# Optimization experiments

Hardware: AMD Instinct MI355X
Metric: run time of the kernel (lower is better)

The kernel has to match this reference:

```python
import jax, jax.numpy as jnp
import numpy as np

N, D_IN, D_OUT = 4096, 1024, 1024

def setup_inputs() -> dict:
    key = jax.random.key(0)
    k1, k2, k3, k4 = jax.random.split(key, 4)
    x = jax.random.normal(k1, (N, D_IN), dtype=jnp.float32)
    # original uses torch.rand (uniform [0,1)) for params
    w_query = jax.random.uniform(k2, (D_IN, D_OUT), dtype=jnp.float32)
    w_key = jax.random.uniform(k3, (D_IN, D_OUT), dtype=jnp.float32)
    w_value = jax.random.uniform(k4, (D_IN, D_OUT), dtype=jnp.float32)
    return {"x": x, "w_query": w_query, "w_key": w_key, "w_value": w_value}

def reference(x, w_query, w_key, w_value):
    queries = x @ w_query          # [N, d_out]
    keys = x @ w_key               # [N, d_out]
    values = x @ w_value           # [N, d_out]
    scale = keys.shape[-1] ** 0.5
    scores = queries @ keys.T      # [N, N]
    attn = jax.nn.softmax(scores / scale, axis=-1)
    return attn @ values           # [N, d_out]
```

## Files before the change

### kernel.cpp

```cpp
#include <hip/hip_runtime.h>
#include <math.h>

#define NROWS 4096
#define DDIM  1024

typedef __attribute__((ext_vector_type(8))) short short8;
typedef __attribute__((ext_vector_type(4))) float f32x4;

__device__ __forceinline__ ushort f2bf(float v) {
  union { float f; uint32_t u; } c; c.f = v;
  uint32_t u = c.u;
  uint32_t lsb = (u >> 16) & 1u;
  u += 0x7fffu + lsb;
  return (ushort)(u >> 16);
}
__device__ __forceinline__ float bf2f(ushort h) {
  union { uint32_t u; float f; } c; c.u = ((uint32_t)h) << 16;
  return c.f;
}

__device__ __forceinline__ void gll16(const void* g, void* l) {
  __builtin_amdgcn_global_load_lds((const __attribute__((address_space(1))) void*)g,
                                   (__attribute__((address_space(3))) void*)l, 16, 0, 0);
}

__device__ __forceinline__ size_t pidx(int r, int c, int ldt) {
  return ((size_t)((r >> 4) * ldt + (c >> 5))) * 512 +
         ((c >> 3) & 3) * 128 + (r & 15) * 8 + (c & 7);
}

__global__ __launch_bounds__(256) void prep(const float* __restrict__ x,
                                            const float* __restrict__ wq,
                                            const float* __restrict__ wk,
                                            const float* __restrict__ wv,
                                            ushort* Xh, ushort* Xl,
                                            ushort* Wqh, ushort* Wql,
                                            ushort* Wkh, ushort* Wkl, ushort* Wvh) {
  __shared__ float tl[32][33];
  const int b = blockIdx.x, t = threadIdx.x;
  if (b < 1024) {
    const float4* src = (const float4*)x;
    ushort4* hi = (ushort4*)Xh;
    ushort4* lo = (ushort4*)Xl;
#pragma unroll
    for (int r = 0; r < 4; ++r) {
      int i = b * 1024 + r * 256 + t;
      float4 v = src[i];
      ushort4 h, l;
      h.x = f2bf(v.x); l.x = f2bf(v.x - bf2f(h.x));
      h.y = f2bf(v.y); l.y = f2bf(v.y - bf2f(h.y));
      h.z = f2bf(v.z); l.z = f2bf(v.z - bf2f(h.z));
      h.w = f2bf(v.w); l.w = f2bf(v.w - bf2f(h.w));
      hi[i] = h; lo[i] = l;
    }
  } else {
    const int z = (b - 1024) >> 10;
    const int tile = (b - 1024) & 1023;
    const float* src = z == 0 ? wq : (z == 1 ? wk : wv);
    ushort* dh = z == 0 ? Wqh : (z == 1 ? Wkh : Wvh);
    ushort* dl = z == 0 ? Wql : (z == 1 ? Wkl : nullptr);
    const int r0 = (tile >> 5) * 32;
    const int c0 = (tile & 31) * 32;
    const int tx = t & 31, ty = t >> 5;
    for (int i = ty; i < 32; i += 8)
      tl[i][tx] = src[(size_t)(r0 + i) * DDIM + c0 + tx];
    __syncthreads();
    for (int i = ty; i < 32; i += 8) {
      float v = tl[tx][i];
      ushort h = f2bf(v);
      size_t o = (size_t)(c0 + i) * DDIM + r0 + tx;
      dh[o] = h;
      if (dl) dl[o] = f2bf(v - bf2f(h));
    }
  }
}

template <int BM, bool SPLIT>
__device__ __forceinline__ void gemm_core(const ushort* __restrict__ Ah,
                                          const ushort* __restrict__ Al,
                                          const ushort* __restrict__ Bh,
                                          const ushort* __restrict__ Bl,
                                          int lda, int ldb, int kbeg, int kend,
                                          int m0, int n0, ushort* sm,
                                          f32x4 (*acc)[4]) {
  constexpr int MI = BM / 32;
  constexpr int ATILE = BM * 32;
  constexpr int BTILE = 128 * 32;
  ushort* sAh = sm;
  ushort* sAl = SPLIT ? sm + ATILE : nullptr;
  ushort* sBh = sm + (SPLIT ? 2 * ATILE : ATILE);
  ushort* sBl = SPLIT ? sBh + BTILE : nullptr;

  const int t = threadIdx.x;
  const int wv = t >> 6, ln = t & 63;
  const int quad = ln >> 4, l16 = ln & 15;
  const int key = (l16 >> 1) & 3;
  const int arb = (wv >> 1) * (BM / 2);
  const int crb = (wv & 1) * 64;

  for (int k0 = kbeg; k0 < kend; k0 += 32) {
#pragma unroll
    for (int r = 0; r < BM * 64 / 4096; ++r) {
      int f = t * 16 + r * 4096;
      int row = f >> 6;
      int srcq = ((f >> 4) & 3) ^ ((row >> 1) & 3);
      size_t go = (size_t)(m0 + row) * lda + k0 + srcq * 8;
      gll16(Ah + go, sAh + (f >> 1));
      if (SPLIT) gll16(Al + go, sAl + (f >> 1));
    }
#pragma unroll
    for (int r = 0; r < 2; ++r) {
      int f = t * 16 + r * 4096;
      int row = f >> 6;
      int srcq = ((f >> 4) & 3) ^ ((row >> 1) & 3);
      size_t go = (size_t)(n0 + row) * ldb + k0 + srcq * 8;
      gll16(Bh + go, sBh + (f >> 1));
      if (SPLIT) gll16(Bl + go, sBl + (f >> 1));
    }
    __syncthreads();

    short8 ah[MI], bh[4], al[MI], bl[4];
#pragma unroll
    for (int i = 0; i < MI; ++i) {
      int off = (arb + i * 16 + l16) * 32 + (quad ^ key) * 8;
      ah[i] = *(const short8*)(sAh + off);
      if (SPLIT) al[i] = *(const short8*)(sAl + off);
    }
#pragma unroll
    for (int j = 0; j < 4; ++j) {
      int off = (crb + j * 16 + l16) * 32 + (quad ^ key) * 8;
      bh[j] = *(const short8*)(sBh + off);
      if (SPLIT) bl[j] = *(const short8*)(sBl + off);
    }
#pragma unroll
    for (int i = 0; i < MI; ++i)
#pragma unroll
      for (int j = 0; j < 4; ++j) {
        acc[i][j] = __builtin_amdgcn_mfma_f32_16x16x32_bf16(ah[i], bh[j], acc[i][j], 0, 0, 0);
        if (SPLIT) {
          acc[i][j] = __builtin_amdgcn_mfma_f32_16x16x32_bf16(ah[i], bl[j], acc[i][j], 0, 0, 0);
          acc[i][j] = __builtin_amdgcn_mfma_f32_16x16x32_bf16(al[i], bh[j], acc[i][j], 0, 0, 0);
        }
      }
    __syncthreads();
  }
}

__global__ __launch_bounds__(256) void gemm_qkv(const ushort* __restrict__ Xh,
                                                const ushort* __restrict__ Xl,
                                                const ushort* __restrict__ Wqh, const ushort* __restrict__ Wql,
                                                const ushort* __restrict__ Wkh, const ushort* __restrict__ Wkl,
                                                const ushort* __restrict__ Wvh,
                                                ushort* Qh, ushort* Ql, ushort* Kh, ushort* Kl, ushort* Vt) {
  extern __shared__ ushort sm[];
  const int which = blockIdx.x % 3;
  const int g = blockIdx.x / 3;
  const int t = threadIdx.x;
  const int wv = t >> 6, ln = t & 63;
  const int quad = ln >> 4, l16 = ln & 15;

  f32x4 acc[4][4];
#pragma unroll
  for (int i = 0; i < 4; ++i)
#pragma unroll
    for (int j = 0; j < 4; ++j) acc[i][j] = (f32x4){0.f, 0.f, 0.f, 0.f};

  if (which == 2) {
    const int m0 = g * 128;
    const int n0 = blockIdx.y * 128;
    gemm_core<128, false>(Wvh, nullptr, Xh, nullptr, DDIM, DDIM, 0, DDIM, m0, n0, sm, acc);
#pragma unroll
    for (int i = 0; i < 4; ++i)
#pragma unroll
      for (int j = 0; j < 4; ++j) {
        int kv = n0 + (wv & 1) * 64 + j * 16 + l16;
        int d = m0 + (wv >> 1) * 64 + i * 16 + quad * 4;
#pragma unroll
        for (int r2 = 0; r2 < 4; ++r2)
          Vt[pidx(d + r2, kv, NROWS / 32)] = f2bf(acc[i][j][r2]);
      }
  } else {
    const int n0 = g * 128;
    const int m0 = blockIdx.y * 128;
    const ushort* Bh = which ? Wkh : Wqh;
    const ushort* Bl = which ? Wkl : Wql;
    gemm_core<128, true>(Xh, Xl, Bh, Bl, DDIM, DDIM, 0, DDIM, m0, n0, sm, acc);
    const float scale = which ? 1.0f : 0.03125f;
    ushort* H = which ? Kh : Qh;
    ushort* L = which ? Kl : Ql;
#pragma unroll
    for (int i = 0; i < 4; ++i)
#pragma unroll
      for (int j = 0; j < 4; ++j) {
        int col = n0 + (wv & 1) * 64 + j * 16 + l16;
        int rw = m0 + (wv >> 1) * 64 + i * 16 + quad * 4;
#pragma unroll
        for (int r2 = 0; r2 < 4; ++r2) {
          float v = acc[i][j][r2] * scale;
          ushort h = f2bf(v);
          size_t o = pidx(rw + r2, col, DDIM / 32);
          H[o] = h;
          L[o] = f2bf(v - bf2f(h));
        }
      }
  }
}

__global__ __launch_bounds__(256) void gemm_s(const ushort* __restrict__ Qh, const ushort* __restrict__ Ql,
                                              const ushort* __restrict__ Kh, const ushort* __restrict__ Kl,
                                              float* __restrict__ S) {
  const int n0 = blockIdx.x * 128, m0 = blockIdx.y * 128;
  const int t = threadIdx.x;
  const int wv = t >> 6, ln = t & 63;
  const int quad = ln >> 4, l16 = ln & 15;
  const int arb = (wv >> 1) * 64, crb = (wv & 1) * 64;
  const int ra = (m0 + arb) >> 4;
  const int rb = (n0 + crb) >> 4;

  f32x4 acc[4][4];
#pragma unroll
  for (int i = 0; i < 4; ++i)
#pragma unroll
    for (int j = 0; j < 4; ++j) acc[i][j] = (f32x4){0.f, 0.f, 0.f, 0.f};

  size_t baseA[4], baseB[4];
#pragma unroll
  for (int i = 0; i < 4; ++i) baseA[i] = (size_t)(ra + i) * 16384 + ln * 8;
#pragma unroll
  for (int j = 0; j < 4; ++j) baseB[j] = (size_t)(rb + j) * 16384 + ln * 8;

#pragma unroll 2
  for (int s = 0; s < 32; ++s) {
    short8 ah[4], al[4];
#pragma unroll
    for (int i = 0; i < 4; ++i) {
      size_t o = baseA[i] + (size_t)s * 512;
      ah[i] = *(const short8*)(Qh + o);
      al[i] = *(const short8*)(Ql + o);
    }
#pragma unroll
    for (int j = 0; j < 4; ++j) {
      size_t o = baseB[j] + (size_t)s * 512;
      short8 bh = *(const short8*)(Kh + o);
      short8 bl = *(const short8*)(Kl + o);
#pragma unroll
      for (int i = 0; i < 4; ++i) {
        acc[i][j] = __builtin_amdgcn_mfma_f32_16x16x32_bf16(ah[i], bh, acc[i][j], 0, 0, 0);
        acc[i][j] = __builtin_amdgcn_mfma_f32_16x16x32_bf16(ah[i], bl, acc[i][j], 0, 0, 0);
        acc[i][j] = __builtin_amdgcn_mfma_f32_16x16x32_bf16(al[i], bh, acc[i][j], 0, 0, 0);
      }
    }
  }

#pragma unroll
  for (int i = 0; i < 4; ++i)
#pragma unroll
    for (int j = 0; j < 4; ++j) {
      int col = n0 + crb + j * 16 + l16;
      int rw = m0 + arb + i * 16 + quad * 4;
#pragma unroll
      for (int r2 = 0; r2 < 4; ++r2)
        S[(size_t)(rw + r2) * NROWS + col] = acc[i][j][r2];
    }
}

__global__ __launch_bounds__(256) void softmax_pack(const float* __restrict__ S,
                                                    ushort* __restrict__ P) {
  const int row = blockIdx.x, t = threadIdx.x;
  const float* Sr = S + (size_t)row * NROWS;
  const float4* S4 = (const float4*)Sr;
  float4 v[4];
  float mx = -3.4e38f;
#pragma unroll
  for (int c = 0; c < 4; ++c) {
    v[c] = S4[c * 256 + t];
    mx = fmaxf(mx, fmaxf(fmaxf(v[c].x, v[c].y), fmaxf(v[c].z, v[c].w)));
  }
  __shared__ float red[4];
  for (int o = 32; o >= 1; o >>= 1) mx = fmaxf(mx, __shfl_xor(mx, o));
  int wv = t >> 6, ln = t & 63;
  if (ln == 0) red[wv] = mx;
  __syncthreads();
  mx = fmaxf(fmaxf(red[0], red[1]), fmaxf(red[2], red[3]));
  float s = 0.f;
#pragma unroll
  for (int c = 0; c < 4; ++c) {
    v[c].x = __expf(v[c].x - mx);
    v[c].y = __expf(v[c].y - mx);
    v[c].z = __expf(v[c].z - mx);
    v[c].w = __expf(v[c].w - mx);
    s += v[c].x + v[c].y + v[c].z + v[c].w;
  }
  for (int o = 32; o >= 1; o >>= 1) s += __shfl_xor(s, o);
  __syncthreads();
  if (ln == 0) red[wv] = s;
  __syncthreads();
  s = red[0] + red[1] + red[2] + red[3];
  float inv = 1.f / s;
#pragma unroll
  for (int c = 0; c < 4; ++c) {
    ushort4 h;
    h.x = f2bf(v[c].x * inv);
    h.y = f2bf(v[c].y * inv);
    h.z = f2bf(v[c].z * inv);
    h.w = f2bf(v[c].w * inv);
    int c0 = 1024 * c + 4 * t;
    *(ushort4*)(P + pidx(row, c0, NROWS / 32)) = h;
  }
}

__global__ __launch_bounds__(256) void gemm_pv(const ushort* __restrict__ P,
                                               const ushort* __restrict__ Vt,
                                               float* __restrict__ Out) {
  const int n0 = blockIdx.x * 128, m0 = blockIdx.y * 64;
  const int t = threadIdx.x;
  const int wv = t >> 6, ln = t & 63;
  const int quad = ln >> 4, l16 = ln & 15;
  const int arb = (wv >> 1) * 32, crb = (wv & 1) * 64;
  const int ra = (m0 + arb) >> 4;
  const int rb = (n0 + crb) >> 4;

  f32x4 acc[2][4];
#pragma unroll
  for (int i = 0; i < 2; ++i)
#pragma unroll
    for (int j = 0; j < 4; ++j) acc[i][j] = (f32x4){0.f, 0.f, 0.f, 0.f};

  size_t baseA[2], baseB[4];
#pragma unroll
  for (int i = 0; i < 2; ++i) baseA[i] = (size_t)(ra + i) * 65536 + ln * 8;
#pragma unroll
  for (int j = 0; j < 4; ++j) baseB[j] = (size_t)(rb + j) * 65536 + ln * 8;

#pragma unroll 2
  for (int s = 0; s < 128; ++s) {
    short8 a0 = *(const short8*)(P + baseA[0] + (size_t)s * 512);
    short8 a1 = *(const short8*)(P + baseA[1] + (size_t)s * 512);
#pragma unroll
    for (int j = 0; j < 4; ++j) {
      short8 b = *(const short8*)(Vt + baseB[j] + (size_t)s * 512);
      acc[0][j] = __builtin_amdgcn_mfma_f32_16x16x32_bf16(a0, b, acc[0][j], 0, 0, 0);
      acc[1][j] = __builtin_amdgcn_mfma_f32_16x16x32_bf16(a1, b, acc[1][j], 0, 0, 0);
    }
  }

#pragma unroll
  for (int i = 0; i < 2; ++i)
#pragma unroll
    for (int j = 0; j < 4; ++j) {
      int col = n0 + crb + j * 16 + l16;
      int rw = m0 + arb + i * 16 + quad * 4;
#pragma unroll
      for (int r2 = 0; r2 < 4; ++r2)
        Out[(size_t)(rw + r2) * DDIM + col] = acc[i][j][r2];
    }
}

extern "C" void kernel_launch(void* const* d_in, const int* in_sizes, int n_in,
                              void* d_out, int out_size, void* d_ws, size_t ws_size,
                              hipStream_t stream) {
  const float* x  = (const float*)d_in[0];
  const float* wq = (const float*)d_in[1];
  const float* wk = (const float*)d_in[2];
  const float* wv = (const float*)d_in[3];
  char* ws = (char*)d_ws;
  const size_t MB = 1u << 20;

  ushort* Vt  = (ushort*)(ws + 0);
  ushort* Qh  = (ushort*)(ws + 8 * MB);
  ushort* Ql  = (ushort*)(ws + 16 * MB);
  ushort* Kh  = (ushort*)(ws + 24 * MB);
  ushort* Kl  = (ushort*)(ws + 32 * MB);
  ushort* Pp  = (ushort*)(ws + 8 * MB);
  ushort* Xh  = (ushort*)(ws + 40 * MB);
  ushort* Xl  = (ushort*)(ws + 48 * MB);
  ushort* Wqh = (ushort*)(ws + 56 * MB);
  ushort* Wql = (ushort*)(ws + 58 * MB);
  ushort* Wkh = (ushort*)(ws + 60 * MB);
  ushort* Wkl = (ushort*)(ws + 62 * MB);
  ushort* Wvh = (ushort*)(ws + 64 * MB);
  float*  S   = (float*)(ws + 40 * MB);
  float*  Out = (float*)d_out;

  prep<<<4096, 256, 0, stream>>>(x, wq, wk, wv, Xh, Xl, Wqh, Wql, Wkh, Wkl, Wvh);
  gemm_qkv<<<dim3(24, 32), 256, 32768, stream>>>(Xh, Xl, Wqh, Wql, Wkh, Wkl, Wvh,
                                                 Qh, Ql, Kh, Kl, Vt);
  gemm_s<<<dim3(32, 32), 256, 0, stream>>>(Qh, Ql, Kh, Kl, S);
  softmax_pack<<<NROWS, 256, 0, stream>>>(S, Pp);
  gemm_pv<<<dim3(8, 64), 256, 0, stream>>>(Pp, Vt, Out);
}
```

Before: 346.6 us.

## Pre-pack X and W into MFMA tile layout and use direct-load GEMM everywhere

```diff
diff --git a/kernel.cpp b/kernel.cpp
--- a/kernel.cpp
+++ b/kernel.cpp
@@ -17,11 +17,6 @@
 __device__ __forceinline__ float bf2f(ushort h) {
   union { uint32_t u; float f; } c; c.u = ((uint32_t)h) << 16;
   return c.f;
-}
-
-__device__ __forceinline__ void gll16(const void* g, void* l) {
-  __builtin_amdgcn_global_load_lds((const __attribute__((address_space(1))) void*)g,
-                                   (__attribute__((address_space(3))) void*)l, 16, 0, 0);
 }
 
 __device__ __forceinline__ size_t pidx(int r, int c, int ldt) {
@@ -40,18 +35,20 @@
   const int b = blockIdx.x, t = threadIdx.x;
   if (b < 1024) {
     const float4* src = (const float4*)x;
-    ushort4* hi = (ushort4*)Xh;
-    ushort4* lo = (ushort4*)Xl;
 #pragma unroll
     for (int r = 0; r < 4; ++r) {
       int i = b * 1024 + r * 256 + t;
+      int row = i >> 8;
+      int c = (i & 255) << 2;
       float4 v = src[i];
       ushort4 h, l;
       h.x = f2bf(v.x); l.x = f2bf(v.x - bf2f(h.x));
       h.y = f2bf(v.y); l.y = f2bf(v.y - bf2f(h.y));
       h.z = f2bf(v.z); l.z = f2bf(v.z - bf2f(h.z));
       h.w = f2bf(v.w); l.w = f2bf(v.w - bf2f(h.w));
-      hi[i] = h; lo[i] = l;
+      size_t o = pidx(row, c, DDIM / 32);
+      *(ushort4*)(Xh + o) = h;
+      *(ushort4*)(Xl + o) = l;
     }
   } else {
     const int z = (b - 1024) >> 10;
@@ -68,81 +65,57 @@
     for (int i = ty; i < 32; i += 8) {
       float v = tl[tx][i];
       ushort h = f2bf(v);
-      size_t o = (size_t)(c0 + i) * DDIM + r0 + tx;
+      size_t o = pidx(c0 + i, r0 + tx, DDIM / 32);
       dh[o] = h;
       if (dl) dl[o] = f2bf(v - bf2f(h));
     }
   }
 }
 
-template <int BM, bool SPLIT>
-__device__ __forceinline__ void gemm_core(const ushort* __restrict__ Ah,
-                                          const ushort* __restrict__ Al,
-                                          const ushort* __restrict__ Bh,
-                                          const ushort* __restrict__ Bl,
-                                          int lda, int ldb, int kbeg, int kend,
-                                          int m0, int n0, ushort* sm,
-                                          f32x4 (*acc)[4]) {
-  constexpr int MI = BM / 32;
-  constexpr int ATILE = BM * 32;
-  constexpr int BTILE = 128 * 32;
-  ushort* sAh = sm;
-  ushort* sAl = SPLIT ? sm + ATILE : nullptr;
-  ushort* sBh = sm + (SPLIT ? 2 * ATILE : ATILE);
-  ushort* sBl = SPLIT ? sBh + BTILE : nullptr;
-
+template <bool SPLIT, int KT>
+__device__ __forceinline__ void direct_gemm(const ushort* __restrict__ Ah,
+                                            const ushort* __restrict__ Al,
+                                            const ushort* __restrict__ Bh,
+                                            const ushort* __restrict__ Bl,
+                                            int m0, int n0, f32x4 (*acc)[4]) {
   const int t = threadIdx.x;
   const int wv = t >> 6, ln = t & 63;
-  const int quad = ln >> 4, l16 = ln & 15;
-  const int key = (l16 >> 1) & 3;
-  const int arb = (wv >> 1) * (BM / 2);
-  const int crb = (wv & 1) * 64;
-
-  for (int k0 = kbeg; k0 < kend; k0 += 32) {
-#pragma unroll
-    for (int r = 0; r < BM * 64 / 4096; ++r) {
-      int f = t * 16 + r * 4096;
-      int row = f >> 6;
-      int srcq = ((f >> 4) & 3) ^ ((row >> 1) & 3);
-      size_t go = (size_t)(m0 + row) * lda + k0 + srcq * 8;
-      gll16(Ah + go, sAh + (f >> 1));
-      if (SPLIT) gll16(Al + go, sAl + (f >> 1));
-    }
-#pragma unroll
-    for (int r = 0; r < 2; ++r) {
-      int f = t * 16 + r * 4096;
-      int row = f >> 6;
-      int srcq = ((f >> 4) & 3) ^ ((row >> 1) & 3);
-      size_t go = (size_t)(n0 + row) * ldb + k0 + srcq * 8;
-      gll16(Bh + go, sBh + (f >> 1));
-      if (SPLIT) gll16(Bl + go, sBl + (f >> 1));
-    }
-    __syncthreads();
-
-    short8 ah[MI], bh[4], al[MI], bl[4];
-#pragma unroll
-    for (int i = 0; i < MI; ++i) {
-      int off = (arb + i * 16 + l16) * 32 + (quad ^ key) * 8;
-      ah[i] = *(const short8*)(sAh + off);
-      if (SPLIT) al[i] = *(const short8*)(sAl + off);
+  const int arb = (wv >> 1) * 64, crb = (wv & 1) * 64;
+  const int ra = (m0 + arb) >> 4;
+  const int rb = (n0 + crb) >> 4;
+  const size_t ts = (size_t)KT * 512;
+
+  size_t baseA[4], baseB[4];
+#pragma unroll
+  for (int i = 0; i < 4; ++i) baseA[i] = (size_t)(ra + i) * ts + ln * 8;
+#pragma unroll
+  for (int j = 0; j < 4; ++j) baseB[j] = (size_t)(rb + j) * ts + ln * 8;
+
+#pragma unroll 2
+  for (int s = 0; s < KT; ++s) {
+    short8 ah[4], al[4];
+#pragma unroll
+    for (int i = 0; i < 4; ++i) {
+      size_t o = baseA[i] + (size_t)s * 512;
+      ah[i] = *(const short8*)(Ah + o);
+      if constexpr (SPLIT) al[i] = *(const short8*)(Al + o);
     }
 #pragma unroll
     for (int j = 0; j < 4; ++j) {
-      int off = (crb + j * 16 + l16) * 32 + (quad ^ key) * 8;
-      bh[j] = *(const short8*)(sBh + off);
-      if (SPLIT) bl[j] = *(const short8*)(sBl + off);
-    }
-#pragma unroll
-    for (int i = 0; i < MI; ++i)
-#pragma unroll
-      for (int j = 0; j < 4; ++j) {
-        acc[i][j] = __builtin_amdgcn_mfma_f32_16x16x32_bf16(ah[i], bh[j], acc[i][j], 0, 0, 0);
-        if (SPLIT) {
-          acc[i][j] = __builtin_amdgcn_mfma_f32_16x16x32_bf16(ah[i], bl[j], acc[i][j], 0, 0, 0);
-          acc[i][j] = __builtin_amdgcn_mfma_f32_16x16x32_bf16(al[i], bh[j], acc[i][j], 0, 0, 0);
+      size_t o = baseB[j] + (size_t)s * 512;
+      short8 bh = *(const short8*)(Bh + o);
+#pragma unroll
+      for (int i = 0; i < 4; ++i)
+        acc[i][j] = __builtin_amdgcn_mfma_f32_16x16x32_bf16(ah[i], bh, acc[i][j], 0, 0, 0);
+      if constexpr (SPLIT) {
+        short8 bl = *(const short8*)(Bl + o);
+#pragma unroll
+        for (int i = 0; i < 4; ++i) {
+          acc[i][j] = __builtin_amdgcn_mfma_f32_16x16x32_bf16(ah[i], bl, acc[i][j], 0, 0, 0);
+          acc[i][j] = __builtin_amdgcn_mfma_f32_16x16x32_bf16(al[i], bh, acc[i][j], 0, 0, 0);
         }
       }
-    __syncthreads();
+    }
   }
 }
 
@@ -152,9 +125,9 @@
                                                 const ushort* __restrict__ Wkh, const ushort* __restrict__ Wkl,
                                                 const ushort* __restrict__ Wvh,
                                                 ushort* Qh, ushort* Ql, ushort* Kh, ushort* Kl, ushort* Vt) {
-  extern __shared__ ushort sm[];
   const int which = blockIdx.x % 3;
   const int g = blockIdx.x / 3;
+  const int by = blockIdx.y;
   const int t = threadIdx.x;
   const int wv = t >> 6, ln = t & 63;
   const int quad = ln >> 4, l16 = ln & 15;
@@ -167,8 +140,8 @@
 
   if (which == 2) {
     const int m0 = g * 128;
-    const int n0 = blockIdx.y * 128;
-    gemm_core<128, false>(Wvh, nullptr, Xh, nullptr, DDIM, DDIM, 0, DDIM, m0, n0, sm, acc);
+    const int n0 = by * 128;
+    direct_gemm<false, DDIM / 32>(Wvh, nullptr, Xh, nullptr, m0, n0, acc);
 #pragma unroll
     for (int i = 0; i < 4; ++i)
 #pragma unroll
@@ -181,10 +154,10 @@
       }
   } else {
     const int n0 = g * 128;
-    const int m0 = blockIdx.y * 128;
+    const int m0 = by * 128;
     const ushort* Bh = which ? Wkh : Wqh;
     const ushort* Bl = which ? Wkl : Wql;
-    gemm_core<128, true>(Xh, Xl, Bh, Bl, DDIM, DDIM, 0, DDIM, m0, n0, sm, acc);
+    direct_gemm<true, DDIM / 32>(Xh, Xl, Bh, Bl, m0, n0, acc);
     const float scale = which ? 1.0f : 0.03125f;
     ushort* H = which ? Kh : Qh;
     ushort* L = which ? Kl : Ql;
@@ -213,9 +186,6 @@
   const int t = threadIdx.x;
   const int wv = t >> 6, ln = t & 63;
   const int quad = ln >> 4, l16 = ln & 15;
-  const int arb = (wv >> 1) * 64, crb = (wv & 1) * 64;
-  const int ra = (m0 + arb) >> 4;
-  const int rb = (n0 + crb) >> 4;
 
   f32x4 acc[4][4];
 #pragma unroll
@@ -223,41 +193,14 @@
 #pragma unroll
     for (int j = 0; j < 4; ++j) acc[i][j] = (f32x4){0.f, 0.f, 0.f, 0.f};
 
-  size_t baseA[4], baseB[4];
-#pragma unroll
-  for (int i = 0; i < 4; ++i) baseA[i] = (size_t)(ra + i) * 16384 + ln * 8;
-#pragma unroll
-  for (int j = 0; j < 4; ++j) baseB[j] = (size_t)(rb + j) * 16384 + ln * 8;
-
-#pragma unroll 2
-  for (int s = 0; s < 32; ++s) {
-    short8 ah[4], al[4];
-#pragma unroll
-    for (int i = 0; i < 4; ++i) {
-      size_t o = baseA[i] + (size_t)s * 512;
-      ah[i] = *(const short8*)(Qh + o);
-      al[i] = *(const short8*)(Ql + o);
-    }
+  direct_gemm<true, DDIM / 32>(Qh, Ql, Kh, Kl, m0, n0, acc);
+
+#pragma unroll
+  for (int i = 0; i < 4; ++i)
 #pragma unroll
     for (int j = 0; j < 4; ++j) {
-      size_t o = baseB[j] + (size_t)s * 512;
-      short8 bh = *(const short8*)(Kh + o);
-      short8 bl = *(const short8*)(Kl + o);
-#pragma unroll
-      for (int i = 0; i < 4; ++i) {
-        acc[i][j] = __builtin_amdgcn_mfma_f32_16x16x32_bf16(ah[i], bh, acc[i][j], 0, 0, 0);
-        acc[i][j] = __builtin_amdgcn_mfma_f32_16x16x32_bf16(ah[i], bl, acc[i][j], 0, 0, 0);
-        acc[i][j] = __builtin_amdgcn_mfma_f32_16x16x32_bf16(al[i], bh, acc[i][j], 0, 0, 0);
-      }
-    }
-  }
-
-#pragma unroll
-  for (int i = 0; i < 4; ++i)
-#pragma unroll
-    for (int j = 0; j < 4; ++j) {
-      int col = n0 + crb + j * 16 + l16;
-      int rw = m0 + arb + i * 16 + quad * 4;
+      int col = n0 + (wv & 1) * 64 + j * 16 + l16;
+      int rw = m0 + (wv >> 1) * 64 + i * 16 + quad * 4;
 #pragma unroll
       for (int r2 = 0; r2 < 4; ++r2)
         S[(size_t)(rw + r2) * NROWS + col] = acc[i][j][r2];
@@ -312,44 +255,25 @@
 __global__ __launch_bounds__(256) void gemm_pv(const ushort* __restrict__ P,
                                                const ushort* __restrict__ Vt,
                                                float* __restrict__ Out) {
-  const int n0 = blockIdx.x * 128, m0 = blockIdx.y * 64;
+  const int n0 = blockIdx.x * 128, m0 = blockIdx.y * 128;
   const int t = threadIdx.x;
   const int wv = t >> 6, ln = t & 63;
   const int quad = ln >> 4, l16 = ln & 15;
-  const int arb = (wv >> 1) * 32, crb = (wv & 1) * 64;
-  const int ra = (m0 + arb) >> 4;
-  const int rb = (n0 + crb) >> 4;
-
-  f32x4 acc[2][4];
-#pragma unroll
-  for (int i = 0; i < 2; ++i)
+
+  f32x4 acc[4][4];
+#pragma unroll
+  for (int i = 0; i < 4; ++i)
 #pragma unroll
     for (int j = 0; j < 4; ++j) acc[i][j] = (f32x4){0.f, 0.f, 0.f, 0.f};
 
-  size_t baseA[2], baseB[4];
-#pragma unroll
-  for (int i = 0; i < 2; ++i) baseA[i] = (size_t)(ra + i) * 65536 + ln * 8;
-#pragma unroll
-  for (int j = 0; j < 4; ++j) baseB[j] = (size_t)(rb + j) * 65536 + ln * 8;
-
-#pragma unroll 2
-  for (int s = 0; s < 128; ++s) {
-    short8 a0 = *(const short8*)(P + baseA[0] + (size_t)s * 512);
-    short8 a1 = *(const short8*)(P + baseA[1] + (size_t)s * 512);
+  direct_gemm<false, NROWS / 32>(P, nullptr, Vt, nullptr, m0, n0, acc);
+
+#pragma unroll
+  for (int i = 0; i < 4; ++i)
 #pragma unroll
     for (int j = 0; j < 4; ++j) {
-      short8 b = *(const short8*)(Vt + baseB[j] + (size_t)s * 512);
-      acc[0][j] = __builtin_amdgcn_mfma_f32_16x16x32_bf16(a0, b, acc[0][j], 0, 0, 0);
-      acc[1][j] = __builtin_amdgcn_mfma_f32_16x16x32_bf16(a1, b, acc[1][j], 0, 0, 0);
-    }
-  }
-
-#pragma unroll
-  for (int i = 0; i < 2; ++i)
-#pragma unroll
-    for (int j = 0; j < 4; ++j) {
-      int col = n0 + crb + j * 16 + l16;
-      int rw = m0 + arb + i * 16 + quad * 4;
+      int col = n0 + (wv & 1) * 64 + j * 16 + l16;
+      int rw = m0 + (wv >> 1) * 64 + i * 16 + quad * 4;
 #pragma unroll
       for (int r2 = 0; r2 < 4; ++r2)
         Out[(size_t)(rw + r2) * DDIM + col] = acc[i][j][r2];
@@ -383,9 +307,9 @@
   float*  Out = (float*)d_out;
 
   prep<<<4096, 256, 0, stream>>>(x, wq, wk, wv, Xh, Xl, Wqh, Wql, Wkh, Wkl, Wvh);
-  gemm_qkv<<<dim3(24, 32), 256, 32768, stream>>>(Xh, Xl, Wqh, Wql, Wkh, Wkl, Wvh,
-                                                 Qh, Ql, Kh, Kl, Vt);
+  gemm_qkv<<<dim3(24, 32), 256, 0, stream>>>(Xh, Xl, Wqh, Wql, Wkh, Wkl, Wvh,
+                                             Qh, Ql, Kh, Kl, Vt);
   gemm_s<<<dim3(32, 32), 256, 0, stream>>>(Qh, Ql, Kh, Kl, S);
   softmax_pack<<<NROWS, 256, 0, stream>>>(S, Pp);
-  gemm_pv<<<dim3(8, 64), 256, 0, stream>>>(Pp, Vt, Out);
-}
+  gemm_pv<<<dim3(8, 32), 256, 0, stream>>>(Pp, Vt, Out);
+}
```

Measured after the change: 345.7 us. Within noise of the previous version (-0.3%).
